# Optimization experiments

Hardware: AMD Instinct MI355X
Metric: run time of the kernel (lower is better)

## Reference

```python
import jax, jax.numpy as jnp
import numpy as np

L = 16            # number of levels
F = 2             # features per level
T = 1 << 17       # hashmap size per level (power of 2)
N_TREES = 8       # forest blocks
N = 2_000_000     # query points
RES = np.array([16, 22, 30, 41, 55, 75, 102, 139, 188, 256, 348, 472, 642, 872, 1184, 1608], dtype=np.int64)
# 8 trilinear corner offsets [8,3]
OFFS = np.stack(np.meshgrid([0, 1], [0, 1], [0, 1], indexing='ij'), axis=-1).reshape(8, 3).astype(np.int32)
PRIMES = (np.uint32(1), np.uint32(2654435761), np.uint32(805459861))


def _hash(coords):
    # coords: [N,8,3] int32 grid corner coords -> [N,8] table index (NGP spatial hash)
    c = coords.astype(jnp.uint32)
    h = (c[..., 0] * PRIMES[0]) ^ (c[..., 1] * PRIMES[1]) ^ (c[..., 2] * PRIMES[2])
    return (h & jnp.uint32(T - 1)).astype(jnp.int32)


def setup_inputs() -> dict:
    key = jax.random.key(0)
    k1, k2, k3 = jax.random.split(key, 3)
    block_x = jax.random.uniform(k1, (N, 3), minval=-1.0, maxval=1.0, dtype=jnp.float32)
    bound = 1e-4
    params = jax.random.uniform(k2, (N_TREES, L, T, F), minval=-bound, maxval=bound, dtype=jnp.float32)
    block_inds = jax.random.randint(k3, (N,), 0, N_TREES)
    return {"block_x": block_x, "params": params, "block_inds": block_inds}


def reference(block_x, params, block_inds):
    # block_x in [-1,1]^3 -> [0,1]^3 (matches `block_x / 2.0 + 0.5` in forward)
    x01 = block_x * 0.5 + 0.5
    offs = jnp.asarray(OFFS)                    # [8,3]
    offs_b = jnp.asarray(OFFS, dtype=bool)      # [8,3]
    outs = []
    for l in range(L):
        R = int(RES[l])
        pos = x01 * (R - 1)                     # [N,3]
        p0 = jnp.floor(pos)
        w = pos - p0                            # trilinear fracs [N,3]
        p0i = p0.astype(jnp.int32)
        corners = jnp.clip(p0i[:, None, :] + offs[None], 0, R - 1)   # [N,8,3]
        idx = _hash(corners)                                          # [N,8]
        feats = params[block_inds[:, None], l, idx, :]                # [N,8,F] per-tree gather
        wc = jnp.prod(jnp.where(offs_b[None], w[:, None, :], 1.0 - w[:, None, :]), axis=-1)  # [N,8]
        outs.append(jnp.einsum('nc,ncf->nf', wc, feats))              # [N,F]
    return jnp.concatenate(outs, axis=-1)        # [N, L*F]
```

## Files before the change

### kernel.cpp

```cpp
#include <hip/hip_runtime.h>

#define NLEVELS 16
#define TSIZE 131072
#define TMASK (TSIZE - 1)
#define NBUCK 32768

typedef float f32x4 __attribute__((ext_vector_type(4)));

__device__ __constant__ float RM1_TAB[16] = {
    15.f, 21.f, 29.f, 40.f, 54.f, 74.f, 101.f, 138.f,
    187.f, 255.f, 347.f, 471.f, 641.f, 871.f, 1183.f, 1607.f
};

constexpr float RM1_C[16] = {
    15.f, 21.f, 29.f, 40.f, 54.f, 74.f, 101.f, 138.f,
    187.f, 255.f, 347.f, 471.f, 641.f, 871.f, 1183.f, 1607.f
};

__device__ __forceinline__ unsigned spread4(unsigned v) {
    v = (v | (v << 4)) & 0x0C3u;
    v = (v | (v << 2)) & 0x249u;
    return v;
}

__device__ __forceinline__ unsigned bucket_key(float x, float y, float z, unsigned tree) {
    const int cx = min(max((int)((x * 0.5f + 0.5f) * 16.f), 0), 15);
    const int cy = min(max((int)((y * 0.5f + 0.5f) * 16.f), 0), 15);
    const int cz = min(max((int)((z * 0.5f + 0.5f) * 16.f), 0), 15);
    const unsigned m = spread4((unsigned)cx) | (spread4((unsigned)cy) << 1)
                     | (spread4((unsigned)cz) << 2);
    return (tree << 12) | m;
}


__global__ __launch_bounds__(256) void k_hist(const float* __restrict__ xs,
                                              const int* __restrict__ inds, int N,
                                              unsigned* __restrict__ hist) {
    const int i = blockIdx.x * 256 + threadIdx.x;
    if (i >= N) return;
    const unsigned key = bucket_key(xs[3 * i], xs[3 * i + 1], xs[3 * i + 2],
                                    (unsigned)(inds[i] & 7));
    atomicAdd(&hist[key], 1u);
}

__global__ __launch_bounds__(1024) void k_scan(const unsigned* __restrict__ hist,
                                               unsigned* __restrict__ cursor) {
    __shared__ unsigned sums[1024];
    const int t = threadIdx.x;
    const int per = NBUCK / 1024;
    unsigned s = 0;
    #pragma unroll
    for (int j = 0; j < per; ++j) s += hist[t * per + j];
    sums[t] = s;
    __syncthreads();
    for (int off = 1; off < 1024; off <<= 1) {
        const unsigned add = (t >= off) ? sums[t - off] : 0u;
        __syncthreads();
        sums[t] += add;
        __syncthreads();
    }
    unsigned run = (t == 0) ? 0u : sums[t - 1];
    #pragma unroll
    for (int j = 0; j < per; ++j) {
        cursor[t * per + j] = run;
        run += hist[t * per + j];
    }
}

__global__ __launch_bounds__(256) void k_scatter(const float* __restrict__ xs,
                                                 const int* __restrict__ inds, int N,
                                                 unsigned* __restrict__ cursor,
                                                 float4* __restrict__ sorted) {
    const int i = blockIdx.x * 256 + threadIdx.x;
    if (i >= N) return;
    const float x = xs[3 * i], y = xs[3 * i + 1], z = xs[3 * i + 2];
    const unsigned tree = (unsigned)(inds[i] & 7);
    const unsigned key = bucket_key(x, y, z, tree);
    const unsigned pos = atomicAdd(&cursor[key], 1u);
    sorted[pos] = make_float4(x, y, z, __uint_as_float(((unsigned)i) | (tree << 24)));
}


template<int L>
__device__ __forceinline__ float2 level_one(const float4 p, int tree,
                                            const float* __restrict__ params) {
    constexpr float rm1 = RM1_C[L];
    constexpr int rmax = (int)rm1;

    const float px = (p.x * 0.5f + 0.5f) * rm1;
    const float py = (p.y * 0.5f + 0.5f) * rm1;
    const float pz = (p.z * 0.5f + 0.5f) * rm1;
    const float fx = floorf(px), fy = floorf(py), fz = floorf(pz);
    const float wx = px - fx, wy = py - fy, wz = pz - fz;
    const int ix = (int)fx, iy = (int)fy, iz = (int)fz;

    const int x0 = min(max(ix, 0), rmax), x1 = min(max(ix + 1, 0), rmax);
    const int y0 = min(max(iy, 0), rmax), y1 = min(max(iy + 1, 0), rmax);
    const int z0 = min(max(iz, 0), rmax), z1 = min(max(iz + 1, 0), rmax);

    const unsigned hx0 = (unsigned)x0;
    const unsigned hx1 = (unsigned)x1;
    const unsigned hy0 = (unsigned)y0 * 2654435761u;
    const unsigned hy1 = (unsigned)y1 * 2654435761u;
    const unsigned hz0 = (unsigned)z0 * 805459861u;
    const unsigned hz1 = (unsigned)z1 * 805459861u;

    const float2* __restrict__ tbl =
        (const float2*)(params + (size_t)(tree * NLEVELS + L) * (TSIZE * 2));

    const unsigned m00 = hy0 ^ hz0;
    const unsigned m01 = hy0 ^ hz1;
    const unsigned m10 = hy1 ^ hz0;
    const unsigned m11 = hy1 ^ hz1;
    const unsigned i000 = (hx0 ^ m00) & TMASK;
    const unsigned i001 = (hx0 ^ m01) & TMASK;
    const unsigned i010 = (hx0 ^ m10) & TMASK;
    const unsigned i011 = (hx0 ^ m11) & TMASK;

    float2 f0, f1, f2, f3, f4, f5, f6, f7;

    const bool pairOK = ((x0 & 1) == 0) && (x1 == x0 + 1);
    if (pairOK) {
        const float4* __restrict__ tbl4 = (const float4*)tbl;
        const float4 q00 = tbl4[i000 >> 1];
        const float4 q01 = tbl4[i001 >> 1];
        const float4 q10 = tbl4[i010 >> 1];
        const float4 q11 = tbl4[i011 >> 1];
        f0 = (i000 & 1) ? make_float2(q00.z, q00.w) : make_float2(q00.x, q00.y);
        f4 = (i000 & 1) ? make_float2(q00.x, q00.y) : make_float2(q00.z, q00.w);
        f1 = (i001 & 1) ? make_float2(q01.z, q01.w) : make_float2(q01.x, q01.y);
        f5 = (i001 & 1) ? make_float2(q01.x, q01.y) : make_float2(q01.z, q01.w);
        f2 = (i010 & 1) ? make_float2(q10.z, q10.w) : make_float2(q10.x, q10.y);
        f6 = (i010 & 1) ? make_float2(q10.x, q10.y) : make_float2(q10.z, q10.w);
        f3 = (i011 & 1) ? make_float2(q11.z, q11.w) : make_float2(q11.x, q11.y);
        f7 = (i011 & 1) ? make_float2(q11.x, q11.y) : make_float2(q11.z, q11.w);
    } else {
        const unsigned i100 = (hx1 ^ m00) & TMASK;
        const unsigned i101 = (hx1 ^ m01) & TMASK;
        const unsigned i110 = (hx1 ^ m10) & TMASK;
        const unsigned i111 = (hx1 ^ m11) & TMASK;
        f0 = tbl[i000]; f1 = tbl[i001];
        f2 = tbl[i010]; f3 = tbl[i011];
        f4 = tbl[i100]; f5 = tbl[i101];
        f6 = tbl[i110]; f7 = tbl[i111];
    }

    const float wx0 = 1.f - wx, wy0 = 1.f - wy, wz0 = 1.f - wz;
    const float w0 = wx0 * wy0 * wz0;
    const float w1 = wx0 * wy0 * wz;
    const float w2 = wx0 * wy  * wz0;
    const float w3 = wx0 * wy  * wz;
    const float w4 = wx  * wy0 * wz0;
    const float w5 = wx  * wy0 * wz;
    const float w6 = wx  * wy  * wz0;
    const float w7 = wx  * wy  * wz;

    float a0 = 0.f, a1 = 0.f;
    a0 = fmaf(w0, f0.x, a0); a1 = fmaf(w0, f0.y, a1);
    a0 = fmaf(w1, f1.x, a0); a1 = fmaf(w1, f1.y, a1);
    a0 = fmaf(w2, f2.x, a0); a1 = fmaf(w2, f2.y, a1);
    a0 = fmaf(w3, f3.x, a0); a1 = fmaf(w3, f3.y, a1);
    a0 = fmaf(w4, f4.x, a0); a1 = fmaf(w4, f4.y, a1);
    a0 = fmaf(w5, f5.x, a0); a1 = fmaf(w5, f5.y, a1);
    a0 = fmaf(w6, f6.x, a0); a1 = fmaf(w6, f6.y, a1);
    a0 = fmaf(w7, f7.x, a0); a1 = fmaf(w7, f7.y, a1);
    return make_float2(a0, a1);
}


__global__ __launch_bounds__(256) void k_all(const float4* __restrict__ sorted,
                                             const float* __restrict__ params,
                                             float4* __restrict__ out4,
                                             int N, int nc) {
    const int b = blockIdx.x;
    const int q = nc >> 3, r = nc & 7;
    const int j = b & 7;
    const int chunk = j * q + min(j, r) + (b >> 3);
    const int i = chunk * 256 + (int)threadIdx.x;
    if (i >= N) return;

    const float4 p = sorted[i];
    const unsigned wbits = __float_as_uint(p.w);
    const int n = (int)(wbits & 0xFFFFFFu);
    const int tree = (int)(wbits >> 24);

    {
        const float2 r0 = level_one<0>(p, tree, params);
        const float2 r1 = level_one<1>(p, tree, params);
        const float2 r2 = level_one<2>(p, tree, params);
        const float2 r3 = level_one<3>(p, tree, params);
        const float2 r4 = level_one<4>(p, tree, params);
        const float2 r5 = level_one<5>(p, tree, params);
        const float2 r6 = level_one<6>(p, tree, params);
        const float2 r7 = level_one<7>(p, tree, params);
        out4[(size_t)n * 8 + 0] = make_float4(r0.x, r0.y, r1.x, r1.y);
        out4[(size_t)n * 8 + 1] = make_float4(r2.x, r2.y, r3.x, r3.y);
        out4[(size_t)n * 8 + 2] = make_float4(r4.x, r4.y, r5.x, r5.y);
        out4[(size_t)n * 8 + 3] = make_float4(r6.x, r6.y, r7.x, r7.y);
    }
    {
        const float2 r0 = level_one<8>(p, tree, params);
        const float2 r1 = level_one<9>(p, tree, params);
        const float2 r2 = level_one<10>(p, tree, params);
        const float2 r3 = level_one<11>(p, tree, params);
        const float2 r4 = level_one<12>(p, tree, params);
        const float2 r5 = level_one<13>(p, tree, params);
        const float2 r6 = level_one<14>(p, tree, params);
        const float2 r7 = level_one<15>(p, tree, params);
        out4[(size_t)n * 8 + 4] = make_float4(r0.x, r0.y, r1.x, r1.y);
        out4[(size_t)n * 8 + 5] = make_float4(r2.x, r2.y, r3.x, r3.y);
        out4[(size_t)n * 8 + 6] = make_float4(r4.x, r4.y, r5.x, r5.y);
        out4[(size_t)n * 8 + 7] = make_float4(r6.x, r6.y, r7.x, r7.y);
    }
}


__global__ __launch_bounds__(256) void lotd_fwd_fused(
    const float* __restrict__ xs, const float* __restrict__ params,
    const int* __restrict__ inds, float* __restrict__ out, int N)
{
    const int g = blockIdx.x * 256 + threadIdx.x;
    const int n = g >> 4;
    if (n >= N) return;
    const int l = g & 15;
    const float rm1 = RM1_TAB[l];
    const int rmax = (int)rm1;
    const float x = xs[3 * n], y = xs[3 * n + 1], z = xs[3 * n + 2];
    const int tree = inds[n];
    const float px = (x * 0.5f + 0.5f) * rm1;
    const float py = (y * 0.5f + 0.5f) * rm1;
    const float pz = (z * 0.5f + 0.5f) * rm1;
    const float fx = floorf(px), fy = floorf(py), fz = floorf(pz);
    const float wx = px - fx, wy = py - fy, wz = pz - fz;
    const int ix = (int)fx, iy = (int)fy, iz = (int)fz;
    const int x0 = min(max(ix, 0), rmax), x1 = min(max(ix + 1, 0), rmax);
    const int y0 = min(max(iy, 0), rmax), y1 = min(max(iy + 1, 0), rmax);
    const int z0 = min(max(iz, 0), rmax), z1 = min(max(iz + 1, 0), rmax);
    const unsigned hx0 = (unsigned)x0, hx1 = (unsigned)x1;
    const unsigned hy0 = (unsigned)y0 * 2654435761u, hy1 = (unsigned)y1 * 2654435761u;
    const unsigned hz0 = (unsigned)z0 * 805459861u,  hz1 = (unsigned)z1 * 805459861u;
    const float2* tbl = (const float2*)(params + (size_t)(tree * NLEVELS + l) * (TSIZE * 2));
    const float2 f000 = tbl[(hx0 ^ hy0 ^ hz0) & TMASK];
    const float2 f001 = tbl[(hx0 ^ hy0 ^ hz1) & TMASK];
    const float2 f010 = tbl[(hx0 ^ hy1 ^ hz0) & TMASK];
    const float2 f011 = tbl[(hx0 ^ hy1 ^ hz1) & TMASK];
    const float2 f100 = tbl[(hx1 ^ hy0 ^ hz0) & TMASK];
    const float2 f101 = tbl[(hx1 ^ hy0 ^ hz1) & TMASK];
    const float2 f110 = tbl[(hx1 ^ hy1 ^ hz0) & TMASK];
    const float2 f111 = tbl[(hx1 ^ hy1 ^ hz1) & TMASK];
    const float wx0 = 1.f - wx, wy0 = 1.f - wy, wz0 = 1.f - wz;
    float a0 = 0.f, a1 = 0.f;
    a0 = fmaf(wx0*wy0*wz0, f000.x, a0); a1 = fmaf(wx0*wy0*wz0, f000.y, a1);
    a0 = fmaf(wx0*wy0*wz , f001.x, a0); a1 = fmaf(wx0*wy0*wz , f001.y, a1);
    a0 = fmaf(wx0*wy *wz0, f010.x, a0); a1 = fmaf(wx0*wy *wz0, f010.y, a1);
    a0 = fmaf(wx0*wy *wz , f011.x, a0); a1 = fmaf(wx0*wy *wz , f011.y, a1);
    a0 = fmaf(wx *wy0*wz0, f100.x, a0); a1 = fmaf(wx *wy0*wz0, f100.y, a1);
    a0 = fmaf(wx *wy0*wz , f101.x, a0); a1 = fmaf(wx *wy0*wz , f101.y, a1);
    a0 = fmaf(wx *wy *wz0, f110.x, a0); a1 = fmaf(wx *wy *wz0, f110.y, a1);
    a0 = fmaf(wx *wy *wz , f111.x, a0); a1 = fmaf(wx *wy *wz , f111.y, a1);
    ((float2*)out)[(size_t)n * 16 + l] = make_float2(a0, a1);
}

extern "C" void kernel_launch(void* const* d_in, const int* in_sizes, int n_in,
                              void* d_out, int out_size, void* d_ws, size_t ws_size,
                              hipStream_t stream) {
    const float* xs     = (const float*)d_in[0];
    const float* params = (const float*)d_in[1];
    const int*   inds   = (const int*)d_in[2];
    float*       out    = (float*)d_out;

    const int N = in_sizes[0] / 3;
    const int nc = (N + 255) / 256;

    const size_t hist_bytes   = (size_t)NBUCK * 4;
    const size_t head_bytes   = 2 * hist_bytes;
    const size_t sorted_bytes = ((size_t)N * 16 + 255) & ~(size_t)255;
    const size_t need = head_bytes + sorted_bytes;

    if (ws_size < need) {
        const int total = N * NLEVELS;
        lotd_fwd_fused<<<(total + 255) / 256, 256, 0, stream>>>(xs, params, inds, out, N);
        return;
    }

    unsigned* hist   = (unsigned*)d_ws;
    unsigned* cursor = (unsigned*)((char*)d_ws + hist_bytes);
    float4*   sorted = (float4*)((char*)d_ws + head_bytes);

    hipMemsetAsync(hist, 0, hist_bytes, stream);
    k_hist<<<nc, 256, 0, stream>>>(xs, inds, N, hist);
    k_scan<<<1, 1024, 0, stream>>>(hist, cursor);
    k_scatter<<<nc, 256, 0, stream>>>(xs, inds, N, cursor, sorted);

    k_all<<<nc, 256, 0, stream>>>(sorted, params, (float4*)out, N, nc);
}
```

Baseline: 815.2 us.

## Split level computation across four grid rows with nontemporal loads and stores

The main kernel now launches a 2D grid where each blockIdx.y handles four of the sixteen levels for every point, instead of one thread doing all sixteen. This raises parallelism and shrinks per-thread register pressure, and it lets the grid rows work on different level tables, which may improve cache locality per row. Point loads and output stores use nontemporal builtins to avoid polluting cache with streaming data. In exchange, each point's sorted record is re-read four times and the per-level work is issued in four separate passes.

```diff
diff --git a/kernel.cpp b/kernel.cpp
--- a/kernel.cpp
+++ b/kernel.cpp
@@ -168,10 +168,22 @@
 }
 
 
-__global__ __launch_bounds__(256) void k_all(const float4* __restrict__ sorted,
-                                             const float* __restrict__ params,
-                                             float4* __restrict__ out4,
-                                             int N, int nc) {
+template<int G>
+__device__ __forceinline__ void quad_levels(const float4 p, int tree,
+                                            const float* __restrict__ params,
+                                            float2& r0, float2& r1,
+                                            float2& r2, float2& r3) {
+    r0 = level_one<4 * G + 0>(p, tree, params);
+    r1 = level_one<4 * G + 1>(p, tree, params);
+    r2 = level_one<4 * G + 2>(p, tree, params);
+    r3 = level_one<4 * G + 3>(p, tree, params);
+}
+
+__global__ __launch_bounds__(256) void k_quad(const float4* __restrict__ sorted,
+                                              const float* __restrict__ params,
+                                              float4* __restrict__ out4,
+                                              int N, int nc) {
+    const int g = blockIdx.y;
     const int b = blockIdx.x;
     const int q = nc >> 3, r = nc & 7;
     const int j = b & 7;
@@ -179,39 +191,23 @@
     const int i = chunk * 256 + (int)threadIdx.x;
     if (i >= N) return;
 
-    const float4 p = sorted[i];
+    const f32x4 pv = __builtin_nontemporal_load((const f32x4*)&sorted[i]);
+    const float4 p = *(const float4*)&pv;
     const unsigned wbits = __float_as_uint(p.w);
     const int n = (int)(wbits & 0xFFFFFFu);
     const int tree = (int)(wbits >> 24);
 
-    {
-        const float2 r0 = level_one<0>(p, tree, params);
-        const float2 r1 = level_one<1>(p, tree, params);
-        const float2 r2 = level_one<2>(p, tree, params);
-        const float2 r3 = level_one<3>(p, tree, params);
-        const float2 r4 = level_one<4>(p, tree, params);
-        const float2 r5 = level_one<5>(p, tree, params);
-        const float2 r6 = level_one<6>(p, tree, params);
-        const float2 r7 = level_one<7>(p, tree, params);
-        out4[(size_t)n * 8 + 0] = make_float4(r0.x, r0.y, r1.x, r1.y);
-        out4[(size_t)n * 8 + 1] = make_float4(r2.x, r2.y, r3.x, r3.y);
-        out4[(size_t)n * 8 + 2] = make_float4(r4.x, r4.y, r5.x, r5.y);
-        out4[(size_t)n * 8 + 3] = make_float4(r6.x, r6.y, r7.x, r7.y);
-    }
-    {
-        const float2 r0 = level_one<8>(p, tree, params);
-        const float2 r1 = level_one<9>(p, tree, params);
-        const float2 r2 = level_one<10>(p, tree, params);
-        const float2 r3 = level_one<11>(p, tree, params);
-        const float2 r4 = level_one<12>(p, tree, params);
-        const float2 r5 = level_one<13>(p, tree, params);
-        const float2 r6 = level_one<14>(p, tree, params);
-        const float2 r7 = level_one<15>(p, tree, params);
-        out4[(size_t)n * 8 + 4] = make_float4(r0.x, r0.y, r1.x, r1.y);
-        out4[(size_t)n * 8 + 5] = make_float4(r2.x, r2.y, r3.x, r3.y);
-        out4[(size_t)n * 8 + 6] = make_float4(r4.x, r4.y, r5.x, r5.y);
-        out4[(size_t)n * 8 + 7] = make_float4(r6.x, r6.y, r7.x, r7.y);
-    }
+    float2 r0, r1, r2, r3;
+    if      (g == 0) quad_levels<0>(p, tree, params, r0, r1, r2, r3);
+    else if (g == 1) quad_levels<1>(p, tree, params, r0, r1, r2, r3);
+    else if (g == 2) quad_levels<2>(p, tree, params, r0, r1, r2, r3);
+    else             quad_levels<3>(p, tree, params, r0, r1, r2, r3);
+
+    const float4 o0 = make_float4(r0.x, r0.y, r1.x, r1.y);
+    const float4 o1 = make_float4(r2.x, r2.y, r3.x, r3.y);
+    const size_t base = (size_t)n * 8 + 2 * g;
+    __builtin_nontemporal_store(*(const f32x4*)&o0, (f32x4*)&out4[base]);
+    __builtin_nontemporal_store(*(const f32x4*)&o1, (f32x4*)&out4[base + 1]);
 }
 
 
@@ -292,5 +288,6 @@
     k_scan<<<1, 1024, 0, stream>>>(hist, cursor);
     k_scatter<<<nc, 256, 0, stream>>>(xs, inds, N, cursor, sorted);
 
-    k_all<<<nc, 256, 0, stream>>>(sorted, params, (float4*)out, N, nc);
-}
+    dim3 grid(nc, 4);
+    k_quad<<<grid, 256, 0, stream>>>(sorted, params, (float4*)out, N, nc);
+}
```

Result: slower. 1.003 ms (+23.0%).
